# Optimization experiments

Hardware: AMD Instinct MI355X
Metric: run time of the kernel (lower is better)

Reference implementation:

```python
import jax, jax.numpy as jnp
import numpy as np
from jax import lax

D_MODEL = 1024
D_STATE = 128
HEADDIM = 64
EXPAND = 2
NGROUPS = 1
CHUNK = 256
D_INNER = EXPAND * D_MODEL          # 2048
D_SSM = D_INNER                      # d_ssm defaults to d_inner
NHEADS = D_SSM // HEADDIM            # 32
CONV_DIM = D_SSM + 2 * NGROUPS * D_STATE   # 2304
D_IN_PROJ = 2 * D_INNER + 2 * NGROUPS * D_STATE + NHEADS  # 4384 -> d_mlp = 0
BATCH = 2
SEQLEN = 2048
EPS = 1e-5


def setup_inputs() -> dict:
    key = jax.random.key(0)
    ks = jax.random.split(key, 9)
    u = jax.random.normal(ks[0], (BATCH, SEQLEN, D_MODEL), jnp.float32)
    # indices into left-padded (len = SEQLEN+1) sequence; 0 selects the zero pad
    conv_indices = jax.random.randint(ks[1], (BATCH, 4 * SEQLEN), 0, SEQLEN + 1)
    W_in = jax.random.normal(ks[2], (D_IN_PROJ, D_MODEL), jnp.float32) / np.sqrt(D_MODEL).astype(np.float32)
    conv_w = jax.random.normal(ks[3], (CONV_DIM, 4), jnp.float32) * 0.2
    conv_b = jax.random.normal(ks[4], (CONV_DIM,), jnp.float32) * 0.02
    # dt_bias init exactly as the module: inverse-softplus of dt in [dt_min, dt_max]
    dt = jnp.exp(jax.random.uniform(ks[5], (NHEADS,), jnp.float32) * (np.log(0.1) - np.log(0.001)) + np.log(0.001))
    dt = jnp.clip(dt, 1e-4)
    dt_bias = dt + jnp.log(-jnp.expm1(-dt))
    A_log = jnp.log(jax.random.uniform(ks[6], (NHEADS,), jnp.float32, minval=1.0, maxval=16.0))
    D = jnp.ones((NHEADS,), jnp.float32)
    norm_w = jnp.ones((D_SSM,), jnp.float32)
    W_out = jax.random.normal(ks[7], (D_MODEL, D_INNER), jnp.float32) / np.sqrt(D_INNER).astype(np.float32)
    return dict(u=u, conv_indices=conv_indices, W_in=W_in, conv_w=conv_w, conv_b=conv_b,
                dt_bias=dt_bias, A_log=A_log, D=D, norm_w=norm_w, W_out=W_out)


def _segsum(x):
    # x: (b, c, h, cs) -> (b, c, h, cs, cs); out[..., t, s] = sum_{k=s+1..t} x[..., k]
    cs = x.shape[-1]
    cx = jnp.cumsum(x, axis=-1)
    diff = cx[..., :, None] - cx[..., None, :]
    mask = jnp.tril(jnp.ones((cs, cs), dtype=bool))
    return jnp.where(mask, diff, -jnp.inf)


def _ssd(x, dt, A, Bh, Ch, D):
    # Mamba2 SSD chunked scan. x:(b,l,h,p), dt:(b,l,h), A:(h,), Bh/Ch:(b,l,h,n), D:(h,)
    b, l, h, p = x.shape
    n = Bh.shape[-1]
    c = l // CHUNK
    xr = x.reshape(b, c, CHUNK, h, p)
    dtr = dt.reshape(b, c, CHUNK, h)
    Br = Bh.reshape(b, c, CHUNK, h, n)
    Cr = Ch.reshape(b, c, CHUNK, h, n)
    dA = dtr * A                                 # (b,c,cs,h)
    Acum = jnp.cumsum(dA, axis=2)                # (b,c,cs,h)
    Lm = jnp.exp(_segsum(jnp.transpose(dA, (0, 1, 3, 2))))  # (b,c,h,cs,cs)
    dtx = xr * dtr[..., None]                    # dt-weighted inputs
    # intra-chunk (diagonal blocks)
    Yd = jnp.einsum('bcthn,bcshn,bchts,bcshp->bcthp', Cr, Br, Lm, dtx)
    # per-chunk final states
    decay_states = jnp.exp(Acum[:, :, -1:, :] - Acum)        # (b,c,cs,h)
    states = jnp.einsum('bcshn,bcsh,bcshp->bchpn', Br, decay_states, dtx)
    chunk_decay = jnp.exp(Acum[:, :, -1, :])     # (b,c,h)
    def step(h_prev, inp):
        dec, st = inp
        return h_prev * dec[..., None, None] + st, h_prev
    init = jnp.zeros((b, h, p, n), x.dtype)
    _, prev = lax.scan(step, init, (jnp.moveaxis(chunk_decay, 1, 0), jnp.moveaxis(states, 1, 0)))
    prev = jnp.moveaxis(prev, 0, 1)              # (b,c,h,p,n): state entering each chunk
    # inter-chunk (off-diagonal) contribution
    Yoff = jnp.einsum('bcthn,bchpn,bcth->bcthp', Cr, prev, jnp.exp(Acum))
    Y = Yd + Yoff + D[None, None, None, :, None] * xr
    return Y.reshape(b, l, h, p)


def reference(u, conv_indices, W_in, conv_w, conv_b, dt_bias, A_log, D, norm_w, W_out):
    b, l, _ = u.shape
    zxbcdt = u @ W_in.T                          # (b,l,4384); d_mlp == 0
    z, xBC, dt_raw = jnp.split(zxbcdt, [D_SSM, D_SSM + CONV_DIM], axis=-1)
    # tree conv: left-pad seq by 1, gather 4 tree positions per output step, depthwise conv k=4 stride=4
    xc = jnp.transpose(xBC, (0, 2, 1))           # (b, conv_dim, l)
    xp = jnp.pad(xc, ((0, 0), (0, 0), (1, 0)))
    idx = jnp.broadcast_to(conv_indices[:, None, :], (b, CONV_DIM, 4 * l))
    g = jnp.take_along_axis(xp, idx, axis=2).reshape(b, CONV_DIM, l, 4)
    conv = jnp.einsum('bclk,ck->bcl', g, conv_w) + conv_b[None, :, None]
    xBC = jax.nn.silu(jnp.transpose(conv, (0, 2, 1)))  # (b,l,conv_dim)
    x, Bm, Cm = jnp.split(xBC, [D_SSM, D_SSM + NGROUPS * D_STATE], axis=-1)
    x = x.reshape(b, l, NHEADS, HEADDIM)
    hpg = NHEADS // NGROUPS
    Bh = jnp.repeat(Bm.reshape(b, l, NGROUPS, D_STATE), hpg, axis=2)
    Ch = jnp.repeat(Cm.reshape(b, l, NGROUPS, D_STATE), hpg, axis=2)
    dt = jax.nn.softplus(dt_raw + dt_bias)       # dt_softplus=True, default dt_limit
    A = -jnp.exp(A_log.astype(jnp.float32))
    y = _ssd(x, dt, A, Bh, Ch, D).reshape(b, l, D_SSM)
    # RMSNormGated, norm_before_gate=False, group_size = d_ssm (ngroups=1)
    yz = y * jax.nn.silu(z)
    var = jnp.mean(jnp.square(yz), axis=-1, keepdims=True)
    y = yz * lax.rsqrt(var + EPS) * norm_w
    return y @ W_out.T
```

## Files before the change

kernel.cpp:

```cpp
#include <hip/hip_runtime.h>

#define BB 2
#define LL 2048
#define DMODEL 1024
#define DSSM 2048
#define NH 32
#define HD 64
#define DST 128
#define CONVD 2304
#define DPROJ 4384
#define CS 64
#define NC 32
#define BLTOT (BB*LL)

typedef short v8s __attribute__((ext_vector_type(8)));
typedef float v4f __attribute__((ext_vector_type(4)));

__device__ __forceinline__ float b2f(unsigned short h) {
  union { unsigned int u; float f; } v; v.u = ((unsigned int)h) << 16; return v.f;
}
__device__ __forceinline__ unsigned short f2b(float f) {
  union { float f; unsigned int u; } v; v.f = f;
  unsigned int u = v.u;
  return (unsigned short)((u + 0x7fffu + ((u >> 16) & 1u)) >> 16);
}
__device__ __forceinline__ v4f mfma16(v8s a, v8s b, v4f c) {
  return __builtin_amdgcn_mfma_f32_16x16x32_bf16(a, b, c, 0, 0, 0);
}
__device__ __forceinline__ void gl_lds16(const unsigned short* g, unsigned short* l) {
  __builtin_amdgcn_global_load_lds(
      (const __attribute__((address_space(1))) void*)(g),
      (__attribute__((address_space(3))) void*)(l), 16, 0, 0);
}

__global__ __launch_bounds__(256) void cvt3_kernel(
    const float* __restrict__ a, unsigned short* __restrict__ oa, int na4,
    const float* __restrict__ b, unsigned short* __restrict__ ob, int nb4,
    const float* __restrict__ c, unsigned short* __restrict__ oc, int nc4)
{
  int i = blockIdx.x * 256 + threadIdx.x;
  const float* src; unsigned short* dst; int j;
  if (i < na4) { src = a; dst = oa; j = i; }
  else if (i < na4 + nb4) { src = b; dst = ob; j = i - na4; }
  else if (i < na4 + nb4 + nc4) { src = c; dst = oc; j = i - na4 - nb4; }
  else return;
  float4 v = ((const float4*)src)[j];
  ushort4 o;
  o.x = f2b(v.x); o.y = f2b(v.y); o.z = f2b(v.z); o.w = f2b(v.w);
  ((ushort4*)dst)[j] = o;
}

template<int OUT_BF16>
__global__ __launch_bounds__(256) void gemm_bt(
    const unsigned short* __restrict__ A, const unsigned short* __restrict__ Bt,
    void* __restrict__ Cout, int M, int N, int K, int ldc)
{
  const int bm = blockIdx.x, bn = blockIdx.y;
  const int tid = threadIdx.x;
  const int wave = tid >> 6, lane = tid & 63;
  const int wm = wave & 1, wn = wave >> 1;
  const int q = lane >> 4, lr = lane & 15;

  __shared__ __align__(16) unsigned short As[128 * 64];
  __shared__ __align__(16) unsigned short Bs[128 * 64];

  v4f acc[4][4];
#pragma unroll
  for (int i = 0; i < 4; i++)
#pragma unroll
    for (int j = 0; j < 4; j++) acc[i][j] = v4f{0.f, 0.f, 0.f, 0.f};

  const int lrow = lane >> 3;
  const int gchunk = (lane & 7) ^ lrow;

  for (int k0 = 0; k0 < K; k0 += 64) {
    __syncthreads();
#pragma unroll
    for (int it = 0; it < 4; ++it) {
      int r = wave * 32 + it * 8 + lrow;
      const unsigned short* ga = A + (size_t)(bm * 128 + r) * K + k0 + gchunk * 8;
      gl_lds16(ga, &As[(wave * 32 + it * 8) * 64]);
      int rb = bn * 128 + r; if (rb >= N) rb = N - 1;
      const unsigned short* gb = Bt + (size_t)rb * K + k0 + gchunk * 8;
      gl_lds16(gb, &Bs[(wave * 32 + it * 8) * 64]);
    }
    __syncthreads();
#pragma unroll
    for (int ks = 0; ks < 64; ks += 32) {
      const int c0 = (ks >> 3) + q;
      v8s af[4], bf[4];
#pragma unroll
      for (int mt = 0; mt < 4; ++mt) {
        int r = wm * 64 + mt * 16 + lr;
        af[mt] = *(const v8s*)&As[r * 64 + ((c0 ^ (r & 7)) << 3)];
      }
#pragma unroll
      for (int nt = 0; nt < 4; ++nt) {
        int r = wn * 64 + nt * 16 + lr;
        bf[nt] = *(const v8s*)&Bs[r * 64 + ((c0 ^ (r & 7)) << 3)];
      }
#pragma unroll
      for (int mt = 0; mt < 4; ++mt)
#pragma unroll
        for (int nt = 0; nt < 4; ++nt)
          acc[mt][nt] = mfma16(af[mt], bf[nt], acc[mt][nt]);
    }
  }
#pragma unroll
  for (int mt = 0; mt < 4; ++mt) {
#pragma unroll
    for (int nt = 0; nt < 4; ++nt) {
      int row = bm * 128 + wm * 64 + mt * 16 + q * 4;
      int col = bn * 128 + wn * 64 + nt * 16 + lr;
      if (col < N) {
#pragma unroll
        for (int r = 0; r < 4; ++r) {
          float v = acc[mt][nt][r];
          if (OUT_BF16) ((unsigned short*)Cout)[(size_t)(row + r) * ldc + col] = f2b(v);
          else          ((float*)Cout)[(size_t)(row + r) * ldc + col] = v;
        }
      }
    }
  }
}

__global__ __launch_bounds__(256) void conv_kernel(
    const unsigned short* __restrict__ C1, const int* __restrict__ cidx,
    const float* __restrict__ convw, const float* __restrict__ convb,
    const float* __restrict__ dtbias,
    unsigned short* __restrict__ x16, unsigned short* __restrict__ Bg16,
    unsigned short* __restrict__ Cg16, float* __restrict__ dtb)
{
  int bl = blockIdx.x;
  int b = bl >> 11;
  int tid = threadIdx.x;
  __shared__ int idxs[4];
  if (tid < 4) idxs[tid] = cidx[b * (4 * LL) + ((bl & 2047) * 4) + tid];
  __syncthreads();
  const unsigned short* rows[4];
#pragma unroll
  for (int k = 0; k < 4; k++) {
    int iv = idxs[k];
    rows[k] = (iv > 0) ? (C1 + (size_t)(b * LL + iv - 1) * DPROJ + DSSM) : (const unsigned short*)0;
  }
  const float4* cw4 = (const float4*)convw;
#pragma unroll
  for (int it = 0; it < 3; ++it) {
    int unit = tid + it * 256;
    if (unit >= CONVD / 4) break;
    int c4 = unit * 4;
    ushort4 rv[4];
#pragma unroll
    for (int k = 0; k < 4; ++k)
      rv[k] = rows[k] ? *(const ushort4*)(rows[k] + c4) : make_ushort4(0, 0, 0, 0);
    float4 w0 = cw4[c4], w1 = cw4[c4 + 1], w2 = cw4[c4 + 2], w3 = cw4[c4 + 3];
    float4 cb = *(const float4*)(convb + c4);
    float a0 = cb.x + b2f(rv[0].x) * w0.x + b2f(rv[1].x) * w0.y + b2f(rv[2].x) * w0.z + b2f(rv[3].x) * w0.w;
    float a1 = cb.y + b2f(rv[0].y) * w1.x + b2f(rv[1].y) * w1.y + b2f(rv[2].y) * w1.z + b2f(rv[3].y) * w1.w;
    float a2 = cb.z + b2f(rv[0].z) * w2.x + b2f(rv[1].z) * w2.y + b2f(rv[2].z) * w2.z + b2f(rv[3].z) * w2.w;
    float a3 = cb.w + b2f(rv[0].w) * w3.x + b2f(rv[1].w) * w3.y + b2f(rv[2].w) * w3.z + b2f(rv[3].w) * w3.w;
    ushort4 o;
    o.x = f2b(a0 / (1.f + __expf(-a0)));
    o.y = f2b(a1 / (1.f + __expf(-a1)));
    o.z = f2b(a2 / (1.f + __expf(-a2)));
    o.w = f2b(a3 / (1.f + __expf(-a3)));
    if (c4 < DSSM)            *(ushort4*)(x16 + (size_t)bl * DSSM + c4) = o;
    else if (c4 < DSSM + DST) *(ushort4*)(Bg16 + (size_t)bl * DST + (c4 - DSSM)) = o;
    else                      *(ushort4*)(Cg16 + (size_t)bl * DST + (c4 - DSSM - DST)) = o;
  }
  if (tid < NH) {
    float raw = b2f(C1[(size_t)bl * DPROJ + DSSM + CONVD + tid]) + dtbias[tid];
    float dtv = (raw > 20.f) ? raw : log1pf(__expf(raw));
    dtb[(size_t)bl * NH + tid] = dtv;
  }
}

__global__ __launch_bounds__(256) void d1_intra(
    const unsigned short* __restrict__ x16, const unsigned short* __restrict__ Bg16,
    const unsigned short* __restrict__ Cg16, const float* __restrict__ dtb,
    const float* __restrict__ A_log,
    unsigned short* __restrict__ y16, unsigned short* __restrict__ statesb,
    float* __restrict__ cdb, float* __restrict__ acumb)
{
  int gid = blockIdx.x;
  int h = gid & 31, ci = (gid >> 5) & 31, b = gid >> 10;
  int tid = threadIdx.x, wave = tid >> 6, lane = tid & 63, q = lane >> 4, lr = lane & 15;

  __shared__ __align__(16) unsigned short BnG[CS * 136];
  __shared__ __align__(16) unsigned short BTw[DST * 72];
  __shared__ __align__(16) unsigned short xT[HD * 72];
  __shared__ float dt_s[CS], ac_s[CS], dec_s[CS];

  const size_t blbase = (size_t)b * LL + ci * CS;
  const size_t chbase = (size_t)(b * NC + ci) * NH + h;
  float Ah = -__expf(A_log[h]);

  if (wave == 0) {
    float d = dtb[(blbase + lane) * NH + h];
    float a = d * Ah;
#pragma unroll
    for (int off = 1; off < 64; off <<= 1) {
      float u = __shfl_up(a, off, 64);
      if (lane >= off) a += u;
    }
    float tot = __shfl(a, 63, 64);
    dt_s[lane] = d;
    ac_s[lane] = a;
    dec_s[lane] = __expf(tot - a);
    acumb[chbase * CS + lane] = a;
    if (lane == 0) cdb[chbase] = __expf(tot);
  }

#pragma unroll
  for (int g = 0; g < 8; ++g) {
    int f = g * 256 + tid;
    int s = f >> 5, c4 = (f & 31) * 4;
    *(ushort4*)&BnG[s * 136 + c4] = *(const ushort4*)(Bg16 + (blbase + s) * DST + c4);
  }
#pragma unroll
  for (int g = 0; g < 4; ++g) {
    int f = g * 256 + tid;
    int s = f >> 4, p4 = (f & 15) * 4;
    ushort4 xv = *(const ushort4*)(x16 + (blbase + s) * DSSM + h * HD + p4);
    xT[(p4 + 0) * 72 + s] = xv.x;
    xT[(p4 + 1) * 72 + s] = xv.y;
    xT[(p4 + 2) * 72 + s] = xv.z;
    xT[(p4 + 3) * 72 + s] = xv.w;
  }
  __syncthreads();

#pragma unroll
  for (int g = 0; g < 4; ++g) {
    int f = g * 256 + tid;
    int n = f >> 3, sg = f & 7;
    int s0 = sg * 8;
    ushort4 lo, hi;
    lo.x = f2b(b2f(BnG[(s0 + 0) * 136 + n]) * dec_s[s0 + 0] * dt_s[s0 + 0]);
    lo.y = f2b(b2f(BnG[(s0 + 1) * 136 + n]) * dec_s[s0 + 1] * dt_s[s0 + 1]);
    lo.z = f2b(b2f(BnG[(s0 + 2) * 136 + n]) * dec_s[s0 + 2] * dt_s[s0 + 2]);
    lo.w = f2b(b2f(BnG[(s0 + 3) * 136 + n]) * dec_s[s0 + 3] * dt_s[s0 + 3]);
    hi.x = f2b(b2f(BnG[(s0 + 4) * 136 + n]) * dec_s[s0 + 4] * dt_s[s0 + 4]);
    hi.y = f2b(b2f(BnG[(s0 + 5) * 136 + n]) * dec_s[s0 + 5] * dt_s[s0 + 5]);
    hi.z = f2b(b2f(BnG[(s0 + 6) * 136 + n]) * dec_s[s0 + 6] * dt_s[s0 + 6]);
    hi.w = f2b(b2f(BnG[(s0 + 7) * 136 + n]) * dec_s[s0 + 7] * dt_s[s0 + 7]);
    *(ushort4*)&BTw[n * 72 + s0] = lo;
    *(ushort4*)&BTw[n * 72 + s0 + 4] = hi;
  }

  v4f accS[4];
#pragma unroll
  for (int i = 0; i < 4; i++) accS[i] = v4f{0.f, 0.f, 0.f, 0.f};
#pragma unroll
  for (int ks = 0; ks < 128; ks += 32) {
    v8s a = *(const v8s*)(Cg16 + (blbase + wave * 16 + lr) * DST + ks + q * 8);
#pragma unroll
    for (int si = 0; si < 4; ++si) {
      v8s bb = *(const v8s*)&BnG[(si * 16 + lr) * 136 + ks + q * 8];
      accS[si] = mfma16(a, bb, accS[si]);
    }
  }
  __syncthreads();

  {
    int tbase = wave * 16 + q * 4;
#pragma unroll
    for (int si = 0; si < 4; ++si) {
      int s = si * 16 + lr;
      float ds = dt_s[s], as = ac_s[s];
#pragma unroll
      for (int r = 0; r < 4; ++r) {
        int tt = tbase + r;
        float g = 0.f;
        if (s <= tt) g = accS[si][r] * __expf(ac_s[tt] - as) * ds;
        BnG[tt * 72 + s] = f2b(g);
      }
    }
  }
  __syncthreads();

  v4f accY[4], accP0[4], accP1[4];
#pragma unroll
  for (int i = 0; i < 4; i++) { accY[i] = v4f{0.f,0.f,0.f,0.f}; accP0[i] = v4f{0.f,0.f,0.f,0.f}; accP1[i] = v4f{0.f,0.f,0.f,0.f}; }
  int n0 = wave * 32, n1 = wave * 32 + 16;
#pragma unroll
  for (int ks = 0; ks < 64; ks += 32) {
    v8s aG  = *(const v8s*)&BnG[(wave * 16 + lr) * 72 + ks + q * 8];
    v8s aB0 = *(const v8s*)&BTw[(n0 + lr) * 72 + ks + q * 8];
    v8s aB1 = *(const v8s*)&BTw[(n1 + lr) * 72 + ks + q * 8];
#pragma unroll
    for (int nt = 0; nt < 4; ++nt) {
      v8s bb = *(const v8s*)&xT[(nt * 16 + lr) * 72 + ks + q * 8];
      accY[nt]  = mfma16(aG,  bb, accY[nt]);
      accP0[nt] = mfma16(aB0, bb, accP0[nt]);
      accP1[nt] = mfma16(aB1, bb, accP1[nt]);
    }
  }

#pragma unroll
  for (int nt = 0; nt < 4; ++nt) {
    int p = nt * 16 + lr;
#pragma unroll
    for (int r = 0; r < 4; ++r) {
      int t = wave * 16 + q * 4 + r;
      y16[(blbase + t) * DSSM + h * HD + p] = f2b(accY[nt][r]);
    }
  }
  size_t sbase = chbase * (DST * HD);
#pragma unroll
  for (int nt = 0; nt < 4; ++nt) {
    int p = nt * 16 + lr;
#pragma unroll
    for (int r = 0; r < 4; ++r) {
      int na = n0 + q * 4 + r;
      int nb = n1 + q * 4 + r;
      statesb[sbase + (size_t)na * HD + p] = f2b(accP0[nt][r]);
      statesb[sbase + (size_t)nb * HD + p] = f2b(accP1[nt][r]);
    }
  }
}

__global__ __launch_bounds__(256) void d2_scan(
    unsigned short* __restrict__ statesb, const float* __restrict__ cdb)
{
  int g = blockIdx.x;
  int part = g & 7, bh = g >> 3;
  int b = bh >> 5, h = bh & 31;
  int tid = threadIdx.x;
  float run[4] = {0.f, 0.f, 0.f, 0.f};
  for (int ci = 0; ci < NC; ++ci) {
    float cd = cdb[(b * NC + ci) * NH + h];
    size_t base = (((size_t)(b * NC + ci) * NH) + h) * (DST * HD) + part * 1024;
#pragma unroll
    for (int i = 0; i < 4; i++) {
      size_t off = base + tid + i * 256;
      float st = b2f(statesb[off]);
      statesb[off] = f2b(run[i]);
      run[i] = run[i] * cd + st;
    }
  }
}

__global__ __launch_bounds__(256) void d3_inter(
    const unsigned short* __restrict__ x16, const unsigned short* __restrict__ Cg16,
    const unsigned short* __restrict__ statesb, const float* __restrict__ acumb,
    const float* __restrict__ Dp, unsigned short* __restrict__ y16)
{
  int gid = blockIdx.x;
  int h = gid & 31, ci = (gid >> 5) & 31, b = gid >> 10;
  int tid = threadIdx.x, wave = tid >> 6, lane = tid & 63, q = lane >> 4, lr = lane & 15;
  __shared__ __align__(16) unsigned short pT[HD * 136];
  __shared__ __align__(16) float ys[CS * 68];
  __shared__ float ea[CS];
  const size_t blbase = (size_t)b * LL + ci * CS;
  const size_t chbase = (size_t)(b * NC + ci) * NH + h;
  if (tid < CS) ea[tid] = __expf(acumb[chbase * CS + tid]);
  size_t sbase = chbase * (DST * HD);
#pragma unroll
  for (int g = 0; g < 8; ++g) {
    int f = g * 256 + tid;
    int n = f >> 4, p4 = (f & 15) * 4;
    ushort4 v = *(const ushort4*)(statesb + sbase + (size_t)n * HD + p4);
    pT[(p4 + 0) * 136 + n] = v.x;
    pT[(p4 + 1) * 136 + n] = v.y;
    pT[(p4 + 2) * 136 + n] = v.z;
    pT[(p4 + 3) * 136 + n] = v.w;
  }
  __syncthreads();
  v4f acc[4];
#pragma unroll
  for (int i = 0; i < 4; i++) acc[i] = v4f{0.f, 0.f, 0.f, 0.f};
#pragma unroll
  for (int ks = 0; ks < 128; ks += 32) {
    v8s a = *(const v8s*)(Cg16 + (blbase + wave * 16 + lr) * DST + ks + q * 8);
#pragma unroll
    for (int nt = 0; nt < 4; ++nt) {
      v8s bb = *(const v8s*)&pT[(nt * 16 + lr) * 136 + ks + q * 8];
      acc[nt] = mfma16(a, bb, acc[nt]);
    }
  }
#pragma unroll
  for (int nt = 0; nt < 4; ++nt) {
#pragma unroll
    for (int r = 0; r < 4; ++r)
      ys[(wave * 16 + q * 4 + r) * 68 + nt * 16 + lr] = acc[nt][r];
  }
  __syncthreads();
  float Dh = Dp[h];
#pragma unroll
  for (int it = 0; it < 2; ++it) {
    int unit = it * 256 + tid;
    int t = unit >> 3, p8 = (unit & 7) * 8;
    float ea_t = ea[t];
    size_t off = (blbase + t) * DSSM + h * HD + p8;
    uint4 yv = *(const uint4*)(y16 + off);
    uint4 xv = *(const uint4*)(x16 + off);
    float4 o0 = *(const float4*)&ys[t * 68 + p8];
    float4 o1 = *(const float4*)&ys[t * 68 + p8 + 4];
    const unsigned int* yu = (const unsigned int*)&yv;
    const unsigned int* xu = (const unsigned int*)&xv;
    const float* ov = (const float*)&o0;
    float oo[8] = {o0.x, o0.y, o0.z, o0.w, o1.x, o1.y, o1.z, o1.w};
    (void)ov;
    unsigned int ro[4];
#pragma unroll
    for (int d = 0; d < 4; ++d) {
      unsigned short y0 = (unsigned short)(yu[d] & 0xffffu), y1 = (unsigned short)(yu[d] >> 16);
      unsigned short x0 = (unsigned short)(xu[d] & 0xffffu), x1 = (unsigned short)(xu[d] >> 16);
      float v0 = b2f(y0) + ea_t * oo[d * 2 + 0] + Dh * b2f(x0);
      float v1 = b2f(y1) + ea_t * oo[d * 2 + 1] + Dh * b2f(x1);
      ro[d] = (unsigned int)f2b(v0) | ((unsigned int)f2b(v1) << 16);
    }
    *(uint4*)(y16 + off) = make_uint4(ro[0], ro[1], ro[2], ro[3]);
  }
}

__global__ __launch_bounds__(256) void norm_kernel(
    const unsigned short* __restrict__ y16, const unsigned short* __restrict__ C1,
    const float* __restrict__ normw, unsigned short* __restrict__ yzn)
{
  int bl = blockIdx.x;
  int tid = threadIdx.x;
  int wave = tid >> 6, lane = tid & 63;
  int c8 = tid * 8;
  uint4 yv = *(const uint4*)(y16 + (size_t)bl * DSSM + c8);
  uint4 zv = *(const uint4*)(C1 + (size_t)bl * DPROJ + c8);
  const unsigned int* yu = (const unsigned int*)&yv;
  const unsigned int* zu = (const unsigned int*)&zv;
  float vals[8];
  float ss = 0.f;
#pragma unroll
  for (int d = 0; d < 4; ++d) {
    unsigned short y0 = (unsigned short)(yu[d] & 0xffffu), y1 = (unsigned short)(yu[d] >> 16);
    unsigned short z0 = (unsigned short)(zu[d] & 0xffffu), z1 = (unsigned short)(zu[d] >> 16);
    float zf0 = b2f(z0), zf1 = b2f(z1);
    float v0 = b2f(y0) * (zf0 / (1.f + __expf(-zf0)));
    float v1 = b2f(y1) * (zf1 / (1.f + __expf(-zf1)));
    vals[d * 2] = v0; vals[d * 2 + 1] = v1;
    ss += v0 * v0 + v1 * v1;
  }
#pragma unroll
  for (int off = 32; off > 0; off >>= 1) ss += __shfl_down(ss, off);
  __shared__ float red[4];
  if (lane == 0) red[wave] = ss;
  __syncthreads();
  float tot = red[0] + red[1] + red[2] + red[3];
  float scale = rsqrtf(tot * (1.f / 2048.f) + 1e-5f);
  float4 w0 = *(const float4*)(normw + c8);
  float4 w1 = *(const float4*)(normw + c8 + 4);
  float ws[8] = {w0.x, w0.y, w0.z, w0.w, w1.x, w1.y, w1.z, w1.w};
  unsigned int ro[4];
#pragma unroll
  for (int d = 0; d < 4; ++d) {
    unsigned short r0 = f2b(vals[d * 2] * scale * ws[d * 2]);
    unsigned short r1 = f2b(vals[d * 2 + 1] * scale * ws[d * 2 + 1]);
    ro[d] = (unsigned int)r0 | ((unsigned int)r1 << 16);
  }
  *(uint4*)(yzn + (size_t)bl * DSSM + c8) = make_uint4(ro[0], ro[1], ro[2], ro[3]);
}

extern "C" void kernel_launch(void* const* d_in, const int* in_sizes, int n_in,
                              void* d_out, int out_size, void* d_ws, size_t ws_size,
                              hipStream_t stream) {
  const float* u      = (const float*)d_in[0];
  const int*   cidx   = (const int*)d_in[1];
  const float* W_in   = (const float*)d_in[2];
  const float* convw  = (const float*)d_in[3];
  const float* convb  = (const float*)d_in[4];
  const float* dtbias = (const float*)d_in[5];
  const float* A_log  = (const float*)d_in[6];
  const float* Dp     = (const float*)d_in[7];
  const float* normw  = (const float*)d_in[8];
  const float* W_out  = (const float*)d_in[9];

  char* w = (char*)d_ws;
  size_t off = 0;
  auto alloc = [&](size_t bytes) { char* p = w + off; off += (bytes + 255) & ~(size_t)255; return p; };
  unsigned short* u16     = (unsigned short*)alloc((size_t)BLTOT * DMODEL * 2);
  unsigned short* Win16   = (unsigned short*)alloc((size_t)DPROJ * DMODEL * 2);
  unsigned short* Wout16  = (unsigned short*)alloc((size_t)DMODEL * DSSM * 2);
  unsigned short* C1      = (unsigned short*)alloc((size_t)BLTOT * DPROJ * 2);
  unsigned short* x16     = (unsigned short*)alloc((size_t)BLTOT * DSSM * 2);
  unsigned short* Bg16    = (unsigned short*)alloc((size_t)BLTOT * DST * 2);
  unsigned short* Cg16    = (unsigned short*)alloc((size_t)BLTOT * DST * 2);
  float*          dtb     = (float*)alloc((size_t)BLTOT * NH * 4);
  float*          acumb   = (float*)alloc((size_t)BB * NC * NH * CS * 4);
  unsigned short* y16     = (unsigned short*)alloc((size_t)BLTOT * DSSM * 2);
  unsigned short* statesb = (unsigned short*)alloc((size_t)BB * NC * NH * DST * HD * 2);
  float*          cdb     = (float*)alloc((size_t)BB * NC * NH * 4);
  unsigned short* yzn     = (unsigned short*)alloc((size_t)BLTOT * DSSM * 2);

  const int na4 = BLTOT * DMODEL / 4, nb4 = DPROJ * DMODEL / 4, nc4 = DMODEL * DSSM / 4;
  cvt3_kernel<<<(na4 + nb4 + nc4 + 255) / 256, 256, 0, stream>>>(
      u, u16, na4, W_in, Win16, nb4, W_out, Wout16, nc4);

  gemm_bt<1><<<dim3(BLTOT / 128, (DPROJ + 127) / 128), 256, 0, stream>>>(
      u16, Win16, C1, BLTOT, DPROJ, DMODEL, DPROJ);
  conv_kernel<<<BLTOT, 256, 0, stream>>>(C1, cidx, convw, convb, dtbias, x16, Bg16, Cg16, dtb);
  d1_intra<<<BB * NC * NH, 256, 0, stream>>>(x16, Bg16, Cg16, dtb, A_log, y16, statesb, cdb, acumb);
  d2_scan<<<BB * NH * 8, 256, 0, stream>>>(statesb, cdb);
  d3_inter<<<BB * NC * NH, 256, 0, stream>>>(x16, Cg16, statesb, acumb, Dp, y16);
  norm_kernel<<<BLTOT, 256, 0, stream>>>(y16, C1, normw, yzn);
  gemm_bt<0><<<dim3(BLTOT / 128, DMODEL / 128), 256, 0, stream>>>(
      yzn, Wout16, (float*)d_out, BLTOT, DMODEL, DSSM, DMODEL);
}
```

Baseline: 272.8 us.

## Transpose chunk-state layout, widen state scan parallelism, narrow out-proj GEMM tile

Chunk states are now stored p-major (transposed) by swapping MFMA operands in the intra-chunk kernel. This lets the inter-chunk kernel load them into LDS with vector stores instead of a scalar transpose. The state scan now uses 32 segments per head, preloading all chunk values per thread to expose more parallelism and memory-level concurrency. The output projection GEMM is templated to a 64-wide N tile so it launches twice as many blocks, at the cost of less reuse per block.

```diff
diff --git a/kernel.cpp b/kernel.cpp
--- a/kernel.cpp
+++ b/kernel.cpp
@@ -50,11 +50,12 @@
   ((ushort4*)dst)[j] = o;
 }
 
-template<int OUT_BF16>
+template<int TN, int OUT_BF16>
 __global__ __launch_bounds__(256) void gemm_bt(
     const unsigned short* __restrict__ A, const unsigned short* __restrict__ Bt,
     void* __restrict__ Cout, int M, int N, int K, int ldc)
 {
+  constexpr int NT = TN / 32;
   const int bm = blockIdx.x, bn = blockIdx.y;
   const int tid = threadIdx.x;
   const int wave = tid >> 6, lane = tid & 63;
@@ -62,13 +63,13 @@
   const int q = lane >> 4, lr = lane & 15;
 
   __shared__ __align__(16) unsigned short As[128 * 64];
-  __shared__ __align__(16) unsigned short Bs[128 * 64];
-
-  v4f acc[4][4];
+  __shared__ __align__(16) unsigned short Bs[TN * 64];
+
+  v4f acc[4][NT];
 #pragma unroll
   for (int i = 0; i < 4; i++)
 #pragma unroll
-    for (int j = 0; j < 4; j++) acc[i][j] = v4f{0.f, 0.f, 0.f, 0.f};
+    for (int j = 0; j < NT; j++) acc[i][j] = v4f{0.f, 0.f, 0.f, 0.f};
 
   const int lrow = lane >> 3;
   const int gchunk = (lane & 7) ^ lrow;
@@ -78,40 +79,43 @@
 #pragma unroll
     for (int it = 0; it < 4; ++it) {
       int r = wave * 32 + it * 8 + lrow;
-      const unsigned short* ga = A + (size_t)(bm * 128 + r) * K + k0 + gchunk * 8;
-      gl_lds16(ga, &As[(wave * 32 + it * 8) * 64]);
-      int rb = bn * 128 + r; if (rb >= N) rb = N - 1;
-      const unsigned short* gb = Bt + (size_t)rb * K + k0 + gchunk * 8;
-      gl_lds16(gb, &Bs[(wave * 32 + it * 8) * 64]);
+      gl_lds16(A + (size_t)(bm * 128 + r) * K + k0 + gchunk * 8,
+               &As[(wave * 32 + it * 8) * 64]);
+    }
+#pragma unroll
+    for (int it = 0; it < TN / 32; ++it) {
+      int rloc = wave * (TN / 4) + it * 8;
+      int rb = bn * TN + rloc + lrow; if (rb >= N) rb = N - 1;
+      gl_lds16(Bt + (size_t)rb * K + k0 + gchunk * 8, &Bs[rloc * 64]);
     }
     __syncthreads();
 #pragma unroll
     for (int ks = 0; ks < 64; ks += 32) {
       const int c0 = (ks >> 3) + q;
-      v8s af[4], bf[4];
+      v8s af[4], bf[NT];
 #pragma unroll
       for (int mt = 0; mt < 4; ++mt) {
         int r = wm * 64 + mt * 16 + lr;
         af[mt] = *(const v8s*)&As[r * 64 + ((c0 ^ (r & 7)) << 3)];
       }
 #pragma unroll
-      for (int nt = 0; nt < 4; ++nt) {
-        int r = wn * 64 + nt * 16 + lr;
+      for (int nt = 0; nt < NT; ++nt) {
+        int r = wn * (TN / 2) + nt * 16 + lr;
         bf[nt] = *(const v8s*)&Bs[r * 64 + ((c0 ^ (r & 7)) << 3)];
       }
 #pragma unroll
       for (int mt = 0; mt < 4; ++mt)
 #pragma unroll
-        for (int nt = 0; nt < 4; ++nt)
+        for (int nt = 0; nt < NT; ++nt)
           acc[mt][nt] = mfma16(af[mt], bf[nt], acc[mt][nt]);
     }
   }
 #pragma unroll
   for (int mt = 0; mt < 4; ++mt) {
 #pragma unroll
-    for (int nt = 0; nt < 4; ++nt) {
+    for (int nt = 0; nt < NT; ++nt) {
       int row = bm * 128 + wm * 64 + mt * 16 + q * 4;
-      int col = bn * 128 + wn * 64 + nt * 16 + lr;
+      int col = bn * TN + wn * (TN / 2) + nt * 16 + lr;
       if (col < N) {
 #pragma unroll
         for (int r = 0; r < 4; ++r) {
@@ -278,21 +282,27 @@
   }
   __syncthreads();
 
-  v4f accY[4], accP0[4], accP1[4];
-#pragma unroll
-  for (int i = 0; i < 4; i++) { accY[i] = v4f{0.f,0.f,0.f,0.f}; accP0[i] = v4f{0.f,0.f,0.f,0.f}; accP1[i] = v4f{0.f,0.f,0.f,0.f}; }
-  int n0 = wave * 32, n1 = wave * 32 + 16;
+  v4f accY[4], accPT[4][2];
+#pragma unroll
+  for (int i = 0; i < 4; i++) {
+    accY[i] = v4f{0.f,0.f,0.f,0.f};
+    accPT[i][0] = v4f{0.f,0.f,0.f,0.f};
+    accPT[i][1] = v4f{0.f,0.f,0.f,0.f};
+  }
+  int nw = wave * 32;
 #pragma unroll
   for (int ks = 0; ks < 64; ks += 32) {
+    v8s xf[4];
+#pragma unroll
+    for (int i = 0; i < 4; ++i) xf[i] = *(const v8s*)&xT[(i * 16 + lr) * 72 + ks + q * 8];
     v8s aG  = *(const v8s*)&BnG[(wave * 16 + lr) * 72 + ks + q * 8];
-    v8s aB0 = *(const v8s*)&BTw[(n0 + lr) * 72 + ks + q * 8];
-    v8s aB1 = *(const v8s*)&BTw[(n1 + lr) * 72 + ks + q * 8];
+    v8s bw0 = *(const v8s*)&BTw[(nw + lr) * 72 + ks + q * 8];
+    v8s bw1 = *(const v8s*)&BTw[(nw + 16 + lr) * 72 + ks + q * 8];
 #pragma unroll
     for (int nt = 0; nt < 4; ++nt) {
-      v8s bb = *(const v8s*)&xT[(nt * 16 + lr) * 72 + ks + q * 8];
-      accY[nt]  = mfma16(aG,  bb, accY[nt]);
-      accP0[nt] = mfma16(aB0, bb, accP0[nt]);
-      accP1[nt] = mfma16(aB1, bb, accP1[nt]);
+      accY[nt] = mfma16(aG, xf[nt], accY[nt]);
+      accPT[nt][0] = mfma16(xf[nt], bw0, accPT[nt][0]);
+      accPT[nt][1] = mfma16(xf[nt], bw1, accPT[nt][1]);
     }
   }
 
@@ -307,14 +317,15 @@
   }
   size_t sbase = chbase * (DST * HD);
 #pragma unroll
-  for (int nt = 0; nt < 4; ++nt) {
-    int p = nt * 16 + lr;
-#pragma unroll
-    for (int r = 0; r < 4; ++r) {
-      int na = n0 + q * 4 + r;
-      int nb = n1 + q * 4 + r;
-      statesb[sbase + (size_t)na * HD + p] = f2b(accP0[nt][r]);
-      statesb[sbase + (size_t)nb * HD + p] = f2b(accP1[nt][r]);
+  for (int mt = 0; mt < 4; ++mt) {
+#pragma unroll
+    for (int nt = 0; nt < 2; ++nt) {
+      int n = nw + nt * 16 + lr;
+#pragma unroll
+      for (int r = 0; r < 4; ++r) {
+        int p = mt * 16 + q * 4 + r;
+        statesb[sbase + (size_t)p * DST + n] = f2b(accPT[mt][nt][r]);
+      }
     }
   }
 }
@@ -323,20 +334,20 @@
     unsigned short* __restrict__ statesb, const float* __restrict__ cdb)
 {
   int g = blockIdx.x;
-  int part = g & 7, bh = g >> 3;
+  int seg = g & 31, bh = g >> 5;
   int b = bh >> 5, h = bh & 31;
-  int tid = threadIdx.x;
-  float run[4] = {0.f, 0.f, 0.f, 0.f};
+  int e = seg * 256 + threadIdx.x;
+  const size_t cstride = (size_t)NH * DST * HD;
+  size_t base = ((size_t)(b * NC) * NH + h) * (DST * HD) + e;
+  unsigned short st[NC];
+#pragma unroll
+  for (int ci = 0; ci < NC; ++ci) st[ci] = statesb[base + ci * cstride];
+  float run = 0.f;
+#pragma unroll
   for (int ci = 0; ci < NC; ++ci) {
     float cd = cdb[(b * NC + ci) * NH + h];
-    size_t base = (((size_t)(b * NC + ci) * NH) + h) * (DST * HD) + part * 1024;
-#pragma unroll
-    for (int i = 0; i < 4; i++) {
-      size_t off = base + tid + i * 256;
-      float st = b2f(statesb[off]);
-      statesb[off] = f2b(run[i]);
-      run[i] = run[i] * cd + st;
-    }
+    statesb[base + ci * cstride] = f2b(run);
+    run = run * cd + b2f(st[ci]);
   }
 }
 
@@ -358,12 +369,8 @@
 #pragma unroll
   for (int g = 0; g < 8; ++g) {
     int f = g * 256 + tid;
-    int n = f >> 4, p4 = (f & 15) * 4;
-    ushort4 v = *(const ushort4*)(statesb + sbase + (size_t)n * HD + p4);
-    pT[(p4 + 0) * 136 + n] = v.x;
-    pT[(p4 + 1) * 136 + n] = v.y;
-    pT[(p4 + 2) * 136 + n] = v.z;
-    pT[(p4 + 3) * 136 + n] = v.w;
+    int p = f >> 5, c4 = (f & 31) * 4;
+    *(ushort4*)&pT[p * 136 + c4] = *(const ushort4*)(statesb + sbase + (size_t)p * DST + c4);
   }
   __syncthreads();
   v4f acc[4];
@@ -398,9 +405,7 @@
     float4 o1 = *(const float4*)&ys[t * 68 + p8 + 4];
     const unsigned int* yu = (const unsigned int*)&yv;
     const unsigned int* xu = (const unsigned int*)&xv;
-    const float* ov = (const float*)&o0;
     float oo[8] = {o0.x, o0.y, o0.z, o0.w, o1.x, o1.y, o1.z, o1.w};
-    (void)ov;
     unsigned int ro[4];
 #pragma unroll
     for (int d = 0; d < 4; ++d) {
@@ -493,13 +498,13 @@
   cvt3_kernel<<<(na4 + nb4 + nc4 + 255) / 256, 256, 0, stream>>>(
       u, u16, na4, W_in, Win16, nb4, W_out, Wout16, nc4);
 
-  gemm_bt<1><<<dim3(BLTOT / 128, (DPROJ + 127) / 128), 256, 0, stream>>>(
+  gemm_bt<128, 1><<<dim3(BLTOT / 128, (DPROJ + 127) / 128), 256, 0, stream>>>(
       u16, Win16, C1, BLTOT, DPROJ, DMODEL, DPROJ);
   conv_kernel<<<BLTOT, 256, 0, stream>>>(C1, cidx, convw, convb, dtbias, x16, Bg16, Cg16, dtb);
   d1_intra<<<BB * NC * NH, 256, 0, stream>>>(x16, Bg16, Cg16, dtb, A_log, y16, statesb, cdb, acumb);
-  d2_scan<<<BB * NH * 8, 256, 0, stream>>>(statesb, cdb);
+  d2_scan<<<BB * NH * 32, 256, 0, stream>>>(statesb, cdb);
   d3_inter<<<BB * NC * NH, 256, 0, stream>>>(x16, Cg16, statesb, acumb, Dp, y16);
   norm_kernel<<<BLTOT, 256, 0, stream>>>(y16, C1, normw, yzn);
-  gemm_bt<0><<<dim3(BLTOT / 128, DMODEL / 128), 256, 0, stream>>>(
+  gemm_bt<64, 0><<<dim3(BLTOT / 128, DMODEL / 64), 256, 0, stream>>>(
       yzn, Wout16, (float*)d_out, BLTOT, DMODEL, DSSM, DMODEL);
 }
```

Result: faster. 263.7 us (-3.3%).
